# Kernel tuning notes

Hardware: AMD Instinct MI355X
Metric: run time of the kernel (lower is better)

## Reference

```python
import jax, jax.numpy as jnp
import numpy as np

B, Ng, C, H, W, Nt, M, P = 4, 8192, 256, 128, 128, 512, 8, 4
Ch = C // M  # 32 channels per head
EPS = 1e-5


def setup_inputs():
    key = jax.random.key(0)
    ks = jax.random.split(key, 12)
    s = 0.02
    def w(k, shape):
        return jax.random.normal(k, shape, jnp.float32) * s
    return {
        "query": jax.random.normal(ks[0], (B, Ng, C), jnp.float32),
        "value": jax.random.normal(ks[1], (B, C, H, W), jnp.float32),
        "reference_points": jax.random.uniform(ks[2], (B, Ng, 2), dtype=jnp.float32),
        "trajectory_points": jax.random.uniform(ks[3], (B, Nt, 2), dtype=jnp.float32),
        "in_proj_w": w(ks[4], (3 * C, C)),
        "in_proj_b": jnp.zeros((3 * C,), jnp.float32),
        "mha_out_w": w(ks[5], (C, C)),
        "mha_out_b": jnp.zeros((C,), jnp.float32),
        "ln_g": jnp.ones((C,), jnp.float32),
        "ln_b": jnp.zeros((C,), jnp.float32),
        "traj_w": w(ks[6], (C, 2)),
        "traj_b": jnp.zeros((C,), jnp.float32),
        "offs_w": w(ks[7], (M * P * 2, C)),
        "offs_b": jnp.zeros((M * P * 2,), jnp.float32),
        "attw_w": w(ks[8], (M * P, C)),
        "attw_b": jnp.zeros((M * P,), jnp.float32),
        "out_w": w(ks[9], (C, C)),
        "out_b": jnp.zeros((C,), jnp.float32),
    }


def _bilinear_sample(imgf, x, y):
    # imgf: (NM, Ch, H*W); x, y: (NM, Lq, P) unnormalized pixel coords
    # grid_sample semantics: bilinear, padding_mode='zeros', align_corners=False
    NM = imgf.shape[0]
    Lq, Pp = x.shape[1], x.shape[2]
    x0 = jnp.floor(x); y0 = jnp.floor(y)
    x1 = x0 + 1.0;     y1 = y0 + 1.0

    def gather(xi, yi):
        valid = (xi >= 0) & (xi < W) & (yi >= 0) & (yi < H)
        xc = jnp.clip(xi, 0, W - 1).astype(jnp.int32)
        yc = jnp.clip(yi, 0, H - 1).astype(jnp.int32)
        idx = (yc * W + xc).reshape(NM, 1, Lq * Pp)
        v = jnp.take_along_axis(imgf, jnp.broadcast_to(idx, (NM, Ch, Lq * Pp)), axis=2)
        return v.reshape(NM, Ch, Lq, Pp), valid.astype(imgf.dtype)

    v00, m00 = gather(x0, y0)
    v01, m01 = gather(x1, y0)
    v10, m10 = gather(x0, y1)
    v11, m11 = gather(x1, y1)
    wx1 = x - x0; wx0 = 1.0 - wx1
    wy1 = y - y0; wy0 = 1.0 - wy1
    out = (v00 * (wx0 * wy0 * m00)[:, None]
         + v01 * (wx1 * wy0 * m01)[:, None]
         + v10 * (wx0 * wy1 * m10)[:, None]
         + v11 * (wx1 * wy1 * m11)[:, None])
    return out  # (NM, Ch, Lq, P)


def reference(query, value, reference_points, trajectory_points,
              in_proj_w, in_proj_b, mha_out_w, mha_out_b, ln_g, ln_b,
              traj_w, traj_b, offs_w, offs_b, attw_w, attw_b, out_w, out_b):
    # trajectory projection: (B,Nt,2) -> (B,Nt,C)
    tf = trajectory_points @ traj_w.T + traj_b

    # guidance cross-attention (nn.MultiheadAttention, eval mode => no dropout)
    wq, wk, wv = jnp.split(in_proj_w, 3, axis=0)
    bq, bk, bv = jnp.split(in_proj_b, 3, axis=0)
    q = (query @ wq.T + bq).reshape(B, Ng, M, Ch)
    k = (tf @ wk.T + bk).reshape(B, Nt, M, Ch)
    v = (tf @ wv.T + bv).reshape(B, Nt, M, Ch)
    scores = jnp.einsum('bqmc,bkmc->bmqk', q, k) / jnp.sqrt(jnp.float32(Ch))
    probs = jax.nn.softmax(scores, axis=-1)
    ctx = jnp.einsum('bmqk,bkmc->bqmc', probs, v).reshape(B, Ng, C)
    ctx = ctx @ mha_out_w.T + mha_out_b

    # residual + LayerNorm
    x = query + ctx
    mu = x.mean(-1, keepdims=True)
    var = ((x - mu) ** 2).mean(-1, keepdims=True)
    gq = (x - mu) / jnp.sqrt(var + EPS) * ln_g + ln_b

    # sampling offsets & softmax attention weights (L=1 level)
    offs = (gq @ offs_w.T + offs_b).reshape(B, Ng, M, 1, P, 2)
    aw = jax.nn.softmax((gq @ attw_w.T + attw_b).reshape(B, Ng, M, P), axis=-1)
    loc = reference_points[:, :, None, None, None, :] + offs  # (B,Ng,M,1,P,2)

    # deformable sampling core (single level)
    grid = 2.0 * loc[:, :, :, 0] - 1.0                   # (B,Ng,M,P,2)
    grid = grid.transpose(0, 2, 1, 3, 4).reshape(B * M, Ng, P, 2)
    gx = (grid[..., 0] + 1.0) * (W * 0.5) - 0.5
    gy = (grid[..., 1] + 1.0) * (H * 0.5) - 0.5
    imgf = value.reshape(B * M, Ch, H * W)               # per-head feature maps
    samp = _bilinear_sample(imgf, gx, gy)                # (B*M,Ch,Ng,P)
    w_att = aw.transpose(0, 2, 1, 3).reshape(B * M, 1, Ng, P)
    out = (samp * w_att).sum(-1)                         # (B*M,Ch,Ng)

    # faithful to source: view(B,M,Ch,Ng).transpose(1,2).contiguous().view(B,Ng,C)
    out = out.reshape(B, M, Ch, Ng).transpose(0, 2, 1, 3).reshape(B, Ng, C)
    return out @ out_w.T + out_b
```

## Files before the change

kernel.cpp:

```cpp
#include <hip/hip_runtime.h>
#include <hip/hip_bf16.h>
#include <stdint.h>

typedef __bf16 bf16_t;
typedef __bf16 bf16x8 __attribute__((ext_vector_type(8)));
typedef __bf16 bf16x4 __attribute__((ext_vector_type(4)));
typedef float f32x4 __attribute__((ext_vector_type(4)));

#define CEXP 0.25506807186679906f

__device__ __forceinline__ float ldf(const void* p, size_t i, int isf) {
  return isf ? ((const float*)p)[i] : (float)((const bf16_t*)p)[i];
}

__device__ __forceinline__ f32x4 mfma16x16x16(bf16x4 a, bf16x4 b, f32x4 c) {
#if __has_builtin(__builtin_amdgcn_mfma_f32_16x16x16_bf16)
  return __builtin_amdgcn_mfma_f32_16x16x16_bf16(a, b, c, 0, 0, 0);
#elif __has_builtin(__builtin_amdgcn_mfma_f32_16x16x16bf16_1k)
  typedef short s16x4 __attribute__((ext_vector_type(4)));
  return __builtin_amdgcn_mfma_f32_16x16x16bf16_1k(
      __builtin_bit_cast(s16x4, a), __builtin_bit_cast(s16x4, b), c, 0, 0, 0);
#else
  asm("v_mfma_f32_16x16x16_bf16 %0, %1, %2, %0" : "+v"(c) : "v"(a), "v"(b));
  return c;
#endif
}

__device__ __forceinline__ void stage16(const bf16_t* g, bf16_t* l) {
  __builtin_amdgcn_global_load_lds((const __attribute__((address_space(1))) void*)g,
                                   (__attribute__((address_space(3))) void*)l, 16, 0, 0);
}

__global__ __launch_bounds__(256) void detect_dtype(const void* q, int* flag) {
  __shared__ int cnt;
  if (threadIdx.x == 0) cnt = 0;
  __syncthreads();
  const uint16_t* u = (const uint16_t*)q;
  const uint16_t v = u[2 * threadIdx.x];
  const int e = (v >> 7) & 0xFF;
  const int weird = (e >= 0x86 || (v != 0 && e <= 0x65)) ? 1 : 0;
  atomicAdd(&cnt, weird);
  __syncthreads();
  if (threadIdx.x == 0) *flag = (cnt >= 64) ? 1 : 0;
}

__global__ __launch_bounds__(256) void convert_weights(
    const void* in_w, const void* in_b, const void* mow, const void* mob,
    const void* outw, const void* outb, bf16_t* __restrict__ blob,
    const int* __restrict__ flag) {
  const int g = (blockIdx.x * 256 + threadIdx.x) * 4;
  if (g >= 328960) return;
  const int isf = *flag;
  const void* src; size_t off;
  if      (g < 196608) { src = in_w; off = g; }
  else if (g < 197376) { src = in_b; off = g - 196608; }
  else if (g < 262912) { src = mow;  off = g - 197376; }
  else if (g < 263168) { src = mob;  off = g - 262912; }
  else if (g < 328704) { src = outw; off = g - 263168; }
  else                 { src = outb; off = g - 328704; }
#pragma unroll
  for (int k = 0; k < 4; k++) blob[g + k] = (bf16_t)ldf(src, off + k, isf);
}

#define TM 128
#define TN 128
#define TKK 64

__global__ __launch_bounds__(256) void gemm_async(
    const bf16_t* __restrict__ A, const bf16_t* __restrict__ W,
    const bf16_t* __restrict__ bias, void* __restrict__ Cout,
    void* __restrict__ Cout2, int Ndim, int Kdim, int mode, float kscale,
    const int* __restrict__ flagp)
{
  __shared__ __align__(16) bf16_t As[TM * TKK];
  __shared__ __align__(16) bf16_t Ws[TN * TKK];
  const int t    = threadIdx.x;
  const int lane = t & 63;
  const int w    = t >> 6;
  const int wm   = (w & 1) * 64;
  const int wn   = (w >> 1) * 64;
  const int q4   = lane >> 4;
  const int r16  = lane & 15;
  const int tm   = blockIdx.x * TM;
  const int tn   = blockIdx.y * TN;

  f32x4 acc[4][4] = {};

  for (int kt = 0; kt < Kdim; kt += TKK) {
    __syncthreads();
#pragma unroll
    for (int r = 0; r < 4; r++) {
      const int L = w * 256 + r * 64 + lane;
      const int R = L >> 3, c = (L & 7) * 8;
      stage16(A + (size_t)(tm + R) * Kdim + kt + c, As + L * 8);
      stage16(W + (size_t)(tn + R) * Kdim + kt + c, Ws + L * 8);
    }
    __syncthreads();
#pragma unroll
    for (int ks = 0; ks < TKK; ks += 32) {
      bf16x8 af[4], bfm[4];
#pragma unroll
      for (int i = 0; i < 4; i++)
        af[i] = *(const bf16x8*)(As + (wm + 16 * i + r16) * TKK + ks + q4 * 8);
#pragma unroll
      for (int j = 0; j < 4; j++)
        bfm[j] = *(const bf16x8*)(Ws + (wn + 16 * j + r16) * TKK + ks + q4 * 8);
#pragma unroll
      for (int i = 0; i < 4; i++)
#pragma unroll
        for (int j = 0; j < 4; j++)
          acc[i][j] = __builtin_amdgcn_mfma_f32_16x16x32_bf16(af[i], bfm[j], acc[i][j], 0, 0, 0);
    }
  }

  const int isf = (mode == 3) ? *flagp : 1;
#pragma unroll
  for (int j = 0; j < 4; j++) {
    const int col = tn + wn + 16 * j + r16;
    const float bv = (float)bias[col];
#pragma unroll
    for (int i = 0; i < 4; i++) {
      const int row0 = tm + wm + 16 * i + q4 * 4;
#pragma unroll
      for (int rr = 0; rr < 4; rr++) {
        const float v = acc[i][j][rr] + bv;
        const size_t off = (size_t)(row0 + rr) * Ndim + col;
        if (mode == 0) {
          ((bf16_t*)Cout)[off] = (bf16_t)(v * kscale);
        } else if (mode == 6) {
          const int rowg = row0 + rr;
          if (col < 256) {
            ((bf16_t*)Cout)[(size_t)rowg * 256 + col] = (bf16_t)(v * kscale);
          } else {
            const int bb = rowg >> 9, tt = rowg & 511;
            const int c2 = col - 256;
            const int mm = c2 >> 5, ch = c2 & 31;
            ((bf16_t*)Cout2)[(((size_t)(bb * 8 + mm) * 32 + ch) << 9) + tt] = (bf16_t)v;
          }
        } else {
          if (isf) ((float*)Cout)[off] = v; else ((bf16_t*)Cout)[off] = (bf16_t)v;
        }
      }
    }
  }
}

__global__ __launch_bounds__(256) void gemm_f32a(
    const float* __restrict__ Ap, const bf16_t* __restrict__ Wf32path_unused,
    const bf16_t* __restrict__ bias, bf16_t* __restrict__ Cout,
    int Ndim, int Kdim, const bf16_t* __restrict__ W, const int* __restrict__ flagp,
    const void* __restrict__ Araw)
{
  __shared__ __align__(16) bf16_t As[TM * TKK];
  __shared__ __align__(16) bf16_t Ws[TN * TKK];
  const int t    = threadIdx.x;
  const int lane = t & 63;
  const int w    = t >> 6;
  const int wm   = (w & 1) * 64;
  const int wn   = (w >> 1) * 64;
  const int q4   = lane >> 4;
  const int r16  = lane & 15;
  const int tm   = blockIdx.x * TM;
  const int tn   = blockIdx.y * TN;
  const int aisf = *flagp;

  f32x4 acc[4][4] = {};
  const int srow = t >> 1;
  const int skb  = (t & 1) * 32;

  for (int kt = 0; kt < Kdim; kt += TKK) {
    __syncthreads();
    if (aisf) {
      const float4* ga = (const float4*)((const float*)Araw + (size_t)(tm + srow) * Kdim + kt + skb);
#pragma unroll
      for (int kk = 0; kk < 8; kk++) {
        const float4 u = ga[kk];
        bf16x4 h = {(bf16_t)u.x, (bf16_t)u.y, (bf16_t)u.z, (bf16_t)u.w};
        *(bf16x4*)(As + srow * TKK + skb + kk * 4) = h;
      }
    } else {
      const uint4* ga = (const uint4*)((const bf16_t*)Araw + (size_t)(tm + srow) * Kdim + kt + skb);
      uint4* la = (uint4*)(As + srow * TKK + skb);
      la[0] = ga[0]; la[1] = ga[1]; la[2] = ga[2]; la[3] = ga[3];
    }
    {
      const uint4* gw = (const uint4*)(W + (size_t)(tn + srow) * Kdim + kt + skb);
      uint4* lw = (uint4*)(Ws + srow * TKK + skb);
      lw[0] = gw[0]; lw[1] = gw[1]; lw[2] = gw[2]; lw[3] = gw[3];
    }
    __syncthreads();
#pragma unroll
    for (int ks = 0; ks < TKK; ks += 32) {
      bf16x8 af[4], bfm[4];
#pragma unroll
      for (int i = 0; i < 4; i++)
        af[i] = *(const bf16x8*)(As + (wm + 16 * i + r16) * TKK + ks + q4 * 8);
#pragma unroll
      for (int j = 0; j < 4; j++)
        bfm[j] = *(const bf16x8*)(Ws + (wn + 16 * j + r16) * TKK + ks + q4 * 8);
#pragma unroll
      for (int i = 0; i < 4; i++)
#pragma unroll
        for (int j = 0; j < 4; j++)
          acc[i][j] = __builtin_amdgcn_mfma_f32_16x16x32_bf16(af[i], bfm[j], acc[i][j], 0, 0, 0);
    }
  }

#pragma unroll
  for (int j = 0; j < 4; j++) {
    const int col = tn + wn + 16 * j + r16;
    const float bv = (float)bias[col];
#pragma unroll
    for (int i = 0; i < 4; i++) {
      const int row0 = tm + wm + 16 * i + q4 * 4;
#pragma unroll
      for (int rr = 0; rr < 4; rr++)
        Cout[(size_t)(row0 + rr) * Ndim + col] = (bf16_t)(acc[i][j][rr] + bv);
    }
  }
}

__global__ __launch_bounds__(256) void tf_kernel(
    const void* __restrict__ tp, const void* __restrict__ tw,
    const void* __restrict__ tb, bf16_t* __restrict__ tf, const int* __restrict__ flag)
{
  const int isf = *flag;
  const int rowb = blockIdx.x;
  const int c = threadIdx.x;
  const float x = ldf(tp, rowb * 2 + 0, isf);
  const float y = ldf(tp, rowb * 2 + 1, isf);
  const float v = x * ldf(tw, c * 2 + 0, isf) + y * ldf(tw, c * 2 + 1, isf) + ldf(tb, c, isf);
  tf[(size_t)rowb * 256 + c] = (bf16_t)v;
}

__global__ __launch_bounds__(256) void attn_kernel(
    const bf16_t* __restrict__ Q, const bf16_t* __restrict__ Kk,
    const bf16_t* __restrict__ Vt, bf16_t* __restrict__ ctx)
{
  const int t = threadIdx.x;
  const int lane = t & 63, w = t >> 6;
  const int q4 = lane >> 4, r16 = lane & 15;
  const int bm = blockIdx.y;
  const int b = bm >> 3, m = bm & 7;
  const int q0 = blockIdx.x * 256 + w * 64;

  bf16x8 qf[4];
#pragma unroll
  for (int qt = 0; qt < 4; qt++)
    qf[qt] = *(const bf16x8*)(Q + ((size_t)(b * 8192 + q0 + qt * 16 + r16) * 256 + m * 32 + q4 * 8));

  f32x4 acc[4][2] = {};
  f32x4 accl[4] = {};
  const bf16x4 ones = {(bf16_t)1.0f, (bf16_t)1.0f, (bf16_t)1.0f, (bf16_t)1.0f};

  const bf16_t* kbase = Kk + (size_t)b * 512 * 256 + m * 32;
  const bf16_t* vbase = Vt + (size_t)bm * 32 * 512;

  for (int k0 = 0; k0 < 512; k0 += 16) {
    const bf16x8 kf  = *(const bf16x8*)(kbase + (size_t)(k0 + r16) * 256 + q4 * 8);
    const bf16x4 vf0 = *(const bf16x4*)(vbase + ((size_t)r16 << 9) + k0 + q4 * 4);
    const bf16x4 vf1 = *(const bf16x4*)(vbase + ((size_t)(16 + r16) << 9) + k0 + q4 * 4);
#pragma unroll
    for (int qt = 0; qt < 4; qt++) {
      f32x4 z = {};
      const f32x4 s = __builtin_amdgcn_mfma_f32_16x16x32_bf16(kf, qf[qt], z, 0, 0, 0);
      bf16x4 p;
#pragma unroll
      for (int rr = 0; rr < 4; rr++) p[rr] = (bf16_t)exp2f(s[rr]);
      acc[qt][0] = mfma16x16x16(vf0, p, acc[qt][0]);
      acc[qt][1] = mfma16x16x16(vf1, p, acc[qt][1]);
      accl[qt]   = mfma16x16x16(ones, p, accl[qt]);
    }
  }

#pragma unroll
  for (int qt = 0; qt < 4; qt++) {
    const float inv = 1.0f / accl[qt][0];
    const size_t row = (size_t)b * 8192 + q0 + qt * 16 + r16;
    bf16x4 o0, o1;
#pragma unroll
    for (int rr = 0; rr < 4; rr++) {
      o0[rr] = (bf16_t)(acc[qt][0][rr] * inv);
      o1[rr] = (bf16_t)(acc[qt][1][rr] * inv);
    }
    *(bf16x4*)(ctx + row * 256 + m * 32 + q4 * 4)      = o0;
    *(bf16x4*)(ctx + row * 256 + m * 32 + 16 + q4 * 4) = o1;
  }
}

__global__ __launch_bounds__(256) void ln_kernel(
    const bf16_t* __restrict__ y2, const void* __restrict__ query,
    const void* __restrict__ g, const void* __restrict__ beta,
    bf16_t* __restrict__ gqh, bf16_t* __restrict__ gql, const int* __restrict__ flag)
{
  const int isf = *flag;
  const int rowb = blockIdx.x * 4 + (threadIdx.x >> 6);
  const int lane = threadIdx.x & 63;
  const size_t base = (size_t)rowb * 256;
  float x[4];
  float s = 0.f;
#pragma unroll
  for (int k = 0; k < 4; k++) {
    const int c = lane + 64 * k;
    x[k] = ldf(query, base + c, isf) + (float)y2[base + c];
    s += x[k];
  }
  for (int d = 1; d < 64; d <<= 1) s += __shfl_xor(s, d, 64);
  const float mu = s * (1.0f / 256.0f);
  float vs = 0.f;
#pragma unroll
  for (int k = 0; k < 4; k++) { const float d = x[k] - mu; vs += d * d; }
  for (int d = 1; d < 64; d <<= 1) vs += __shfl_xor(vs, d, 64);
  const float rstd = rsqrtf(vs * (1.0f / 256.0f) + 1e-5f);
#pragma unroll
  for (int k = 0; k < 4; k++) {
    const int c = lane + 64 * k;
    const float gv = (x[k] - mu) * rstd * ldf(g, c, isf) + ldf(beta, c, isf);
    const bf16_t hi = (bf16_t)gv;
    gqh[base + c] = hi;
    gql[base + c] = (bf16_t)(gv - (float)hi);
  }
}

__global__ __launch_bounds__(256) void prep_wpad(
    const void* __restrict__ offs_w, const void* __restrict__ attw_w,
    const void* __restrict__ offs_b, const void* __restrict__ attw_b,
    bf16_t* __restrict__ Wph, bf16_t* __restrict__ Wpl, bf16_t* __restrict__ bp,
    const int* __restrict__ flag)
{
  const int isf = *flag;
  const int idx = blockIdx.x * 256 + threadIdx.x;
  const int rowp = idx >> 8, c = idx & 255;
  float v = 0.0f;
  if (rowp < 64)      v = ldf(offs_w, rowp * 256 + c, isf);
  else if (rowp < 96) v = ldf(attw_w, (rowp - 64) * 256 + c, isf);
  const bf16_t hi = (bf16_t)v;
  Wph[idx] = hi;
  Wpl[idx] = (bf16_t)(v - (float)hi);
  if (idx < 128) {
    float bv = 0.0f;
    if (idx < 64)      bv = ldf(offs_b, idx, isf);
    else if (idx < 96) bv = ldf(attw_b, idx - 64, isf);
    bp[idx] = (bf16_t)bv;
  }
}

__global__ __launch_bounds__(256) void gemm_offs(
    const bf16_t* __restrict__ Ahg, const bf16_t* __restrict__ Alg,
    const bf16_t* __restrict__ Whg, const bf16_t* __restrict__ Wlg,
    const bf16_t* __restrict__ bias, float* __restrict__ Cout)
{
  __shared__ __align__(16) bf16_t Ah[128 * 64];
  __shared__ __align__(16) bf16_t Al[128 * 64];
  __shared__ __align__(16) bf16_t Wh[128 * 64];
  __shared__ __align__(16) bf16_t Wl[128 * 64];
  const int t    = threadIdx.x;
  const int lane = t & 63;
  const int w    = t >> 6;
  const int wm   = (w & 1) * 64;
  const int wn   = (w >> 1) * 64;
  const int q4   = lane >> 4;
  const int r16  = lane & 15;
  const int tm   = blockIdx.x * 128;

  f32x4 acc[4][4] = {};
  const int srow = t >> 1;
  const int skb  = (t & 1) * 32;

  for (int kt = 0; kt < 256; kt += 64) {
    __syncthreads();
    {
      const uint4* g0 = (const uint4*)(Ahg + (size_t)(tm + srow) * 256 + kt + skb);
      uint4* l0 = (uint4*)(Ah + srow * 64 + skb);
      l0[0] = g0[0]; l0[1] = g0[1]; l0[2] = g0[2]; l0[3] = g0[3];
      const uint4* g1 = (const uint4*)(Alg + (size_t)(tm + srow) * 256 + kt + skb);
      uint4* l1 = (uint4*)(Al + srow * 64 + skb);
      l1[0] = g1[0]; l1[1] = g1[1]; l1[2] = g1[2]; l1[3] = g1[3];
      const uint4* g2 = (const uint4*)(Whg + (size_t)srow * 256 + kt + skb);
      uint4* l2 = (uint4*)(Wh + srow * 64 + skb);
      l2[0] = g2[0]; l2[1] = g2[1]; l2[2] = g2[2]; l2[3] = g2[3];
      const uint4* g3 = (const uint4*)(Wlg + (size_t)srow * 256 + kt + skb);
      uint4* l3 = (uint4*)(Wl + srow * 64 + skb);
      l3[0] = g3[0]; l3[1] = g3[1]; l3[2] = g3[2]; l3[3] = g3[3];
    }
    __syncthreads();
#pragma unroll
    for (int ks = 0; ks < 64; ks += 32) {
      bf16x8 ah[4], al[4], bh[4], bl[4];
#pragma unroll
      for (int i = 0; i < 4; i++) {
        ah[i] = *(const bf16x8*)(Ah + (wm + 16 * i + r16) * 64 + ks + q4 * 8);
        al[i] = *(const bf16x8*)(Al + (wm + 16 * i + r16) * 64 + ks + q4 * 8);
      }
#pragma unroll
      for (int j = 0; j < 4; j++) {
        bh[j] = *(const bf16x8*)(Wh + (wn + 16 * j + r16) * 64 + ks + q4 * 8);
        bl[j] = *(const bf16x8*)(Wl + (wn + 16 * j + r16) * 64 + ks + q4 * 8);
      }
#pragma unroll
      for (int i = 0; i < 4; i++)
#pragma unroll
        for (int j = 0; j < 4; j++) {
          f32x4 a = acc[i][j];
          a = __builtin_amdgcn_mfma_f32_16x16x32_bf16(al[i], bh[j], a, 0, 0, 0);
          a = __builtin_amdgcn_mfma_f32_16x16x32_bf16(ah[i], bl[j], a, 0, 0, 0);
          a = __builtin_amdgcn_mfma_f32_16x16x32_bf16(ah[i], bh[j], a, 0, 0, 0);
          acc[i][j] = a;
        }
    }
  }

#pragma unroll
  for (int j = 0; j < 4; j++) {
    const int col = wn + 16 * j + r16;
    const float bv = (float)bias[col];
#pragma unroll
    for (int i = 0; i < 4; i++) {
      const int row0 = tm + wm + 16 * i + q4 * 4;
#pragma unroll
      for (int rr = 0; rr < 4; rr++)
        Cout[(size_t)(row0 + rr) * 128 + col] = acc[i][j][rr] + bv;
    }
  }
}

__global__ __launch_bounds__(256) void transpose_value(
    const void* __restrict__ V, bf16_t* __restrict__ Vp, const int* __restrict__ flag)
{
  __shared__ bf16_t tile[32][130];
  const int isf = *flag;
  const int bid = blockIdx.x;
  const int h = bid & 127;
  const int bm = bid >> 7;
  const int b = bm >> 3, mm = bm & 7;
  const int t = threadIdx.x;
  for (int idx = t; idx < 32 * 128; idx += 256) {
    const int ch = idx >> 7, ww = idx & 127;
    tile[ch][ww] = (bf16_t)ldf(V, (((size_t)b * 256 + mm * 32 + ch) * 128 + h) * 128 + ww, isf);
  }
  __syncthreads();
  const size_t base = ((size_t)bm * 128 + h) * 4096;
  for (int idx = t; idx < 32 * 128; idx += 256) {
    const int ww = idx >> 5, ch = idx & 31;
    Vp[base + idx] = tile[ch][ww];
  }
}

__global__ __launch_bounds__(256) void sampler(
    const float* __restrict__ ys, const void* __restrict__ refp,
    const bf16_t* __restrict__ vperm, bf16_t* __restrict__ outs,
    const int* __restrict__ flag)
{
  const int isf = *flag;
  const int t = threadIdx.x;
  const int qt = blockIdx.x;
  const int bm = blockIdx.y;
  const int b = bm >> 3, m = bm & 7;
  const int qq = qt * 256 + t;
  const size_t row = (size_t)b * 8192 + qq;
  const float* y = ys + row * 128;
  const float rx = ldf(refp, row * 2 + 0, isf);
  const float ry = ldf(refp, row * 2 + 1, isf);

  const float l0 = y[64 + m * 4 + 0], l1 = y[64 + m * 4 + 1];
  const float l2 = y[64 + m * 4 + 2], l3 = y[64 + m * 4 + 3];
  const float mx = fmaxf(fmaxf(l0, l1), fmaxf(l2, l3));
  const float e0 = __expf(l0 - mx), e1 = __expf(l1 - mx);
  const float e2 = __expf(l2 - mx), e3 = __expf(l3 - mx);
  const float inv = 1.0f / (e0 + e1 + e2 + e3);
  const float aw[4] = {e0 * inv, e1 * inv, e2 * inv, e3 * inv};

  float acc[32];
#pragma unroll
  for (int ch = 0; ch < 32; ch++) acc[ch] = 0.0f;

  const bf16_t* vbase = vperm + (size_t)bm * (128 * 128 * 32);

  for (int p = 0; p < 4; p++) {
    const float gx = (rx + y[m * 8 + p * 2 + 0]) * 128.0f - 0.5f;
    const float gy = (ry + y[m * 8 + p * 2 + 1]) * 128.0f - 0.5f;
    const float x0f = floorf(gx), y0f = floorf(gy);
    const int x0 = (int)x0f, y0i = (int)y0f;
    const float wx1 = gx - x0f, wx0 = 1.0f - wx1;
    const float wy1 = gy - y0f, wy0 = 1.0f - wy1;
    const float a = aw[p];
    for (int cy = 0; cy < 2; cy++) {
      const int yy = y0i + cy;
      if (yy < 0 || yy >= 128) continue;
      const float wy = cy ? wy1 : wy0;
      for (int cx = 0; cx < 2; cx++) {
        const int xx = x0 + cx;
        if (xx < 0 || xx >= 128) continue;
        const float wgt = a * wy * (cx ? wx1 : wx0);
        const bf16x8* src8 = (const bf16x8*)(vbase + ((size_t)yy * 128 + xx) * 32);
#pragma unroll
        for (int vv = 0; vv < 4; vv++) {
          const bf16x8 d = src8[vv];
#pragma unroll
          for (int e = 0; e < 8; e++) acc[vv * 8 + e] += wgt * (float)d[e];
        }
      }
    }
  }

  const size_t obase = (size_t)b * 8192;
#pragma unroll
  for (int ch = 0; ch < 32; ch++) {
    const size_t orow = obase + (size_t)(ch * 8 + m) * 32 + qt;
    outs[orow * 256 + t] = (bf16_t)acc[ch];
  }
}

extern "C" void kernel_launch(void* const* d_in, const int* in_sizes, int n_in,
                              void* d_out, int out_size, void* d_ws, size_t ws_size,
                              hipStream_t stream) {
  const void* query = d_in[0];
  const void* value = d_in[1];
  const void* refp  = d_in[2];
  const void* trajp = d_in[3];
  const void* in_w  = d_in[4];
  const void* in_b  = d_in[5];
  const void* mow   = d_in[6];
  const void* mob   = d_in[7];
  const void* lng   = d_in[8];
  const void* lnb   = d_in[9];
  const void* tw    = d_in[10];
  const void* tb    = d_in[11];
  const void* ow    = d_in[12];
  const void* ob    = d_in[13];
  const void* aww   = d_in[14];
  const void* awb   = d_in[15];
  const void* outw  = d_in[16];
  const void* outb  = d_in[17];

  char* base = (char*)d_ws;
  float*  ysamp = (float*)(base);
  bf16_t* qout  = (bf16_t*)(base + 16777216);
  bf16_t* ctx   = (bf16_t*)(base + 33554432);
  bf16_t* y2    = (bf16_t*)(base + 50331648);
  bf16_t* tf_ws = (bf16_t*)(base + 67108864);
  bf16_t* k_ws  = (bf16_t*)(base + 68157440);
  bf16_t* vt_g  = (bf16_t*)(base + 69206016);
  bf16_t* blob  = (bf16_t*)(base + 70254592);
  int*    flag  = (int*)(base + 70254592 + 1048560);

  bf16_t* gqh   = qout;
  bf16_t* gql   = ctx;
  bf16_t* vperm = (bf16_t*)(base + 16777216);
  bf16_t* outs  = y2;

  bf16_t* inw_bf  = blob;
  bf16_t* inb_bf  = blob + 196608;
  bf16_t* mow_bf  = blob + 197376;
  bf16_t* mob_bf  = blob + 262912;
  bf16_t* outw_bf = blob + 263168;
  bf16_t* outb_bf = blob + 328704;
  bf16_t* wph     = blob + 328960;
  bf16_t* wpl     = blob + 361728;
  bf16_t* bpad    = blob + 394496;

  detect_dtype<<<dim3(1), dim3(256), 0, stream>>>(query, flag);
  convert_weights<<<dim3(322), dim3(256), 0, stream>>>(in_w, in_b, mow, mob, outw, outb, blob, flag);
  tf_kernel<<<dim3(2048), dim3(256), 0, stream>>>(trajp, tw, tb, tf_ws, flag);
  gemm_async<<<dim3(16, 4), dim3(256), 0, stream>>>(
      tf_ws, inw_bf + 65536, inb_bf + 256, (void*)k_ws, (void*)vt_g, 512, 256, 6, CEXP, flag);
  gemm_f32a<<<dim3(256, 2), dim3(256), 0, stream>>>(
      (const float*)query, nullptr, inb_bf, qout, 256, 256, inw_bf, flag, query);
  attn_kernel<<<dim3(32, 32), dim3(256), 0, stream>>>(qout, k_ws, vt_g, ctx);
  gemm_async<<<dim3(256, 2), dim3(256), 0, stream>>>(
      ctx, mow_bf, mob_bf, (void*)y2, nullptr, 256, 256, 0, 1.0f, flag);
  ln_kernel<<<dim3(8192), dim3(256), 0, stream>>>(y2, query, lng, lnb, gqh, gql, flag);
  prep_wpad<<<dim3(128), dim3(256), 0, stream>>>(ow, aww, ob, awb, wph, wpl, bpad, flag);
  gemm_offs<<<dim3(256, 1), dim3(256), 0, stream>>>(gqh, gql, wph, wpl, bpad, ysamp);
  transpose_value<<<dim3(4096), dim3(256), 0, stream>>>(value, vperm, flag);
  sampler<<<dim3(32, 32), dim3(256), 0, stream>>>(ysamp, refp, vperm, outs, flag);
  gemm_async<<<dim3(256, 2), dim3(256), 0, stream>>>(
      outs, outw_bf, outb_bf, d_out, nullptr, 256, 256, 3, 1.0f, flag);
}
```

Before: 385.6 us.

## Merge prep kernels, inline dtype detection, halve attention tile and prefetch K/V

Replaces the separate dtype-detect, weight-convert, trajectory-feature and offset-weight prep kernels with one prep_all launch. Each kernel now detects the input dtype in-wave with a ballot instead of reading a flag from memory. The attention kernel handles 32 queries per wave over twice as many blocks, prefetches the next K/V fragments across iterations, and packs exp2 results to bf16 with a bit trick. Together these aim to cut launch count and the serial dependency on the flag, and to raise attention occupancy and latency hiding. The risk is a slightly different rounding path for the probabilities.

```diff
diff --git a/kernel.cpp b/kernel.cpp
--- a/kernel.cpp
+++ b/kernel.cpp
@@ -13,16 +13,39 @@
   return isf ? ((const float*)p)[i] : (float)((const bf16_t*)p)[i];
 }
 
+__device__ __forceinline__ int detect_isf(const void* q) {
+  const uint16_t* u = (const uint16_t*)q;
+  const int lane = threadIdx.x & 63;
+  const uint16_t v = u[2 * lane];
+  const int e = (v >> 7) & 0xFF;
+  const int weird = (e >= 0x86 || (v != 0 && e <= 0x65)) ? 1 : 0;
+  return (__popcll(__ballot(weird)) >= 16) ? 1 : 0;
+}
+
+__device__ __forceinline__ float fexp2(float x) {
+#if __has_builtin(__builtin_amdgcn_exp2f)
+  return __builtin_amdgcn_exp2f(x);
+#else
+  return exp2f(x);
+#endif
+}
+
+__device__ __forceinline__ bf16x4 pack4(const f32x4 s) {
+  union { float f; uint32_t u; } a0, a1, a2, a3;
+  a0.f = fexp2(s[0]); a1.f = fexp2(s[1]); a2.f = fexp2(s[2]); a3.f = fexp2(s[3]);
+  uint2 r;
+  r.x = __builtin_amdgcn_perm(a1.u + 0x8000u, a0.u + 0x8000u, 0x07060302u);
+  r.y = __builtin_amdgcn_perm(a3.u + 0x8000u, a2.u + 0x8000u, 0x07060302u);
+  return __builtin_bit_cast(bf16x4, r);
+}
+
 __device__ __forceinline__ f32x4 mfma16x16x16(bf16x4 a, bf16x4 b, f32x4 c) {
 #if __has_builtin(__builtin_amdgcn_mfma_f32_16x16x16_bf16)
   return __builtin_amdgcn_mfma_f32_16x16x16_bf16(a, b, c, 0, 0, 0);
-#elif __has_builtin(__builtin_amdgcn_mfma_f32_16x16x16bf16_1k)
+#else
   typedef short s16x4 __attribute__((ext_vector_type(4)));
   return __builtin_amdgcn_mfma_f32_16x16x16bf16_1k(
       __builtin_bit_cast(s16x4, a), __builtin_bit_cast(s16x4, b), c, 0, 0, 0);
-#else
-  asm("v_mfma_f32_16x16x16_bf16 %0, %1, %2, %0" : "+v"(c) : "v"(a), "v"(b));
-  return c;
 #endif
 }
 
@@ -31,35 +54,52 @@
                                    (__attribute__((address_space(3))) void*)l, 16, 0, 0);
 }
 
-__global__ __launch_bounds__(256) void detect_dtype(const void* q, int* flag) {
-  __shared__ int cnt;
-  if (threadIdx.x == 0) cnt = 0;
-  __syncthreads();
-  const uint16_t* u = (const uint16_t*)q;
-  const uint16_t v = u[2 * threadIdx.x];
-  const int e = (v >> 7) & 0xFF;
-  const int weird = (e >= 0x86 || (v != 0 && e <= 0x65)) ? 1 : 0;
-  atomicAdd(&cnt, weird);
-  __syncthreads();
-  if (threadIdx.x == 0) *flag = (cnt >= 64) ? 1 : 0;
-}
-
-__global__ __launch_bounds__(256) void convert_weights(
+__global__ __launch_bounds__(256) void prep_all(
+    const void* __restrict__ query,
     const void* in_w, const void* in_b, const void* mow, const void* mob,
-    const void* outw, const void* outb, bf16_t* __restrict__ blob,
-    const int* __restrict__ flag) {
-  const int g = (blockIdx.x * 256 + threadIdx.x) * 4;
-  if (g >= 328960) return;
-  const int isf = *flag;
-  const void* src; size_t off;
-  if      (g < 196608) { src = in_w; off = g; }
-  else if (g < 197376) { src = in_b; off = g - 196608; }
-  else if (g < 262912) { src = mow;  off = g - 197376; }
-  else if (g < 263168) { src = mob;  off = g - 262912; }
-  else if (g < 328704) { src = outw; off = g - 263168; }
-  else                 { src = outb; off = g - 328704; }
-#pragma unroll
-  for (int k = 0; k < 4; k++) blob[g + k] = (bf16_t)ldf(src, off + k, isf);
+    const void* outw, const void* outb,
+    const void* trajp, const void* tw, const void* tb,
+    const void* offs_w, const void* attw_w, const void* offs_b, const void* attw_b,
+    bf16_t* __restrict__ blob, bf16_t* __restrict__ tf,
+    bf16_t* __restrict__ Wph, bf16_t* __restrict__ Wpl, bf16_t* __restrict__ bp)
+{
+  const int isf = detect_isf(query);
+  const int bid = blockIdx.x;
+  if (bid < 322) {
+    const int g = (bid * 256 + threadIdx.x) * 4;
+    if (g >= 328960) return;
+    const void* src; size_t off;
+    if      (g < 196608) { src = in_w; off = g; }
+    else if (g < 197376) { src = in_b; off = g - 196608; }
+    else if (g < 262912) { src = mow;  off = g - 197376; }
+    else if (g < 263168) { src = mob;  off = g - 262912; }
+    else if (g < 328704) { src = outw; off = g - 263168; }
+    else                 { src = outb; off = g - 328704; }
+#pragma unroll
+    for (int k = 0; k < 4; k++) blob[g + k] = (bf16_t)ldf(src, off + k, isf);
+  } else if (bid < 322 + 2048) {
+    const int rowb = bid - 322;
+    const int c = threadIdx.x;
+    const float x = ldf(trajp, rowb * 2 + 0, isf);
+    const float y = ldf(trajp, rowb * 2 + 1, isf);
+    const float v = x * ldf(tw, c * 2 + 0, isf) + y * ldf(tw, c * 2 + 1, isf) + ldf(tb, c, isf);
+    tf[(size_t)rowb * 256 + c] = (bf16_t)v;
+  } else {
+    const int idx = (bid - 2370) * 256 + threadIdx.x;
+    const int rowp = idx >> 8, c = idx & 255;
+    float v = 0.0f;
+    if (rowp < 64)      v = ldf(offs_w, rowp * 256 + c, isf);
+    else if (rowp < 96) v = ldf(attw_w, (rowp - 64) * 256 + c, isf);
+    const bf16_t hi = (bf16_t)v;
+    Wph[idx] = hi;
+    Wpl[idx] = (bf16_t)(v - (float)hi);
+    if (idx < 128) {
+      float bv = 0.0f;
+      if (idx < 64)      bv = ldf(offs_b, idx, isf);
+      else if (idx < 96) bv = ldf(attw_b, idx - 64, isf);
+      bp[idx] = (bf16_t)bv;
+    }
+  }
 }
 
 #define TM 128
@@ -70,7 +110,7 @@
     const bf16_t* __restrict__ A, const bf16_t* __restrict__ W,
     const bf16_t* __restrict__ bias, void* __restrict__ Cout,
     void* __restrict__ Cout2, int Ndim, int Kdim, int mode, float kscale,
-    const int* __restrict__ flagp)
+    const void* __restrict__ qdet)
 {
   __shared__ __align__(16) bf16_t As[TM * TKK];
   __shared__ __align__(16) bf16_t Ws[TN * TKK];
@@ -113,7 +153,7 @@
     }
   }
 
-  const int isf = (mode == 3) ? *flagp : 1;
+  const int isf = (mode == 3) ? detect_isf(qdet) : 1;
 #pragma unroll
   for (int j = 0; j < 4; j++) {
     const int col = tn + wn + 16 * j + r16;
@@ -126,7 +166,7 @@
         const float v = acc[i][j][rr] + bv;
         const size_t off = (size_t)(row0 + rr) * Ndim + col;
         if (mode == 0) {
-          ((bf16_t*)Cout)[off] = (bf16_t)(v * kscale);
+          ((bf16_t*)Cout)[off] = (bf16_t)v;
         } else if (mode == 6) {
           const int rowg = row0 + rr;
           if (col < 256) {
@@ -146,10 +186,9 @@
 }
 
 __global__ __launch_bounds__(256) void gemm_f32a(
-    const float* __restrict__ Ap, const bf16_t* __restrict__ Wf32path_unused,
+    const void* __restrict__ Araw, const bf16_t* __restrict__ W,
     const bf16_t* __restrict__ bias, bf16_t* __restrict__ Cout,
-    int Ndim, int Kdim, const bf16_t* __restrict__ W, const int* __restrict__ flagp,
-    const void* __restrict__ Araw)
+    int Ndim, int Kdim, const void* __restrict__ qdet)
 {
   __shared__ __align__(16) bf16_t As[TM * TKK];
   __shared__ __align__(16) bf16_t Ws[TN * TKK];
@@ -162,7 +201,7 @@
   const int r16  = lane & 15;
   const int tm   = blockIdx.x * TM;
   const int tn   = blockIdx.y * TN;
-  const int aisf = *flagp;
+  const int aisf = detect_isf(qdet);
 
   f32x4 acc[4][4] = {};
   const int srow = t >> 1;
@@ -220,19 +259,6 @@
   }
 }
 
-__global__ __launch_bounds__(256) void tf_kernel(
-    const void* __restrict__ tp, const void* __restrict__ tw,
-    const void* __restrict__ tb, bf16_t* __restrict__ tf, const int* __restrict__ flag)
-{
-  const int isf = *flag;
-  const int rowb = blockIdx.x;
-  const int c = threadIdx.x;
-  const float x = ldf(tp, rowb * 2 + 0, isf);
-  const float y = ldf(tp, rowb * 2 + 1, isf);
-  const float v = x * ldf(tw, c * 2 + 0, isf) + y * ldf(tw, c * 2 + 1, isf) + ldf(tb, c, isf);
-  tf[(size_t)rowb * 256 + c] = (bf16_t)v;
-}
-
 __global__ __launch_bounds__(256) void attn_kernel(
     const bf16_t* __restrict__ Q, const bf16_t* __restrict__ Kk,
     const bf16_t* __restrict__ Vt, bf16_t* __restrict__ ctx)
@@ -242,39 +268,44 @@
   const int q4 = lane >> 4, r16 = lane & 15;
   const int bm = blockIdx.y;
   const int b = bm >> 3, m = bm & 7;
-  const int q0 = blockIdx.x * 256 + w * 64;
-
-  bf16x8 qf[4];
-#pragma unroll
-  for (int qt = 0; qt < 4; qt++)
+  const int q0 = blockIdx.x * 128 + w * 32;
+
+  bf16x8 qf[2];
+#pragma unroll
+  for (int qt = 0; qt < 2; qt++)
     qf[qt] = *(const bf16x8*)(Q + ((size_t)(b * 8192 + q0 + qt * 16 + r16) * 256 + m * 32 + q4 * 8));
 
-  f32x4 acc[4][2] = {};
-  f32x4 accl[4] = {};
+  f32x4 acc[2][2] = {};
+  f32x4 accl[2] = {};
   const bf16x4 ones = {(bf16_t)1.0f, (bf16_t)1.0f, (bf16_t)1.0f, (bf16_t)1.0f};
 
-  const bf16_t* kbase = Kk + (size_t)b * 512 * 256 + m * 32;
-  const bf16_t* vbase = Vt + (size_t)bm * 32 * 512;
+  const bf16_t* kbase  = Kk + (size_t)b * 512 * 256 + m * 32 + (size_t)r16 * 256 + q4 * 8;
+  const bf16_t* vbase0 = Vt + (size_t)bm * 32 * 512 + ((size_t)r16 << 9) + q4 * 4;
+  const bf16_t* vbase1 = vbase0 + (16 << 9);
+
+  bf16x8 kf = *(const bf16x8*)(kbase);
+  bf16x4 v0 = *(const bf16x4*)(vbase0);
+  bf16x4 v1 = *(const bf16x4*)(vbase1);
 
   for (int k0 = 0; k0 < 512; k0 += 16) {
-    const bf16x8 kf  = *(const bf16x8*)(kbase + (size_t)(k0 + r16) * 256 + q4 * 8);
-    const bf16x4 vf0 = *(const bf16x4*)(vbase + ((size_t)r16 << 9) + k0 + q4 * 4);
-    const bf16x4 vf1 = *(const bf16x4*)(vbase + ((size_t)(16 + r16) << 9) + k0 + q4 * 4);
-#pragma unroll
-    for (int qt = 0; qt < 4; qt++) {
+    const int nxt = (k0 + 16) & 511;
+    const bf16x8 kf_n = *(const bf16x8*)(kbase + (size_t)nxt * 256);
+    const bf16x4 v0_n = *(const bf16x4*)(vbase0 + nxt);
+    const bf16x4 v1_n = *(const bf16x4*)(vbase1 + nxt);
+#pragma unroll
+    for (int qt = 0; qt < 2; qt++) {
       f32x4 z = {};
       const f32x4 s = __builtin_amdgcn_mfma_f32_16x16x32_bf16(kf, qf[qt], z, 0, 0, 0);
-      bf16x4 p;
-#pragma unroll
-      for (int rr = 0; rr < 4; rr++) p[rr] = (bf16_t)exp2f(s[rr]);
-      acc[qt][0] = mfma16x16x16(vf0, p, acc[qt][0]);
-      acc[qt][1] = mfma16x16x16(vf1, p, acc[qt][1]);
+      const bf16x4 p = pack4(s);
+      acc[qt][0] = mfma16x16x16(v0, p, acc[qt][0]);
+      acc[qt][1] = mfma16x16x16(v1, p, acc[qt][1]);
       accl[qt]   = mfma16x16x16(ones, p, accl[qt]);
     }
-  }
-
-#pragma unroll
-  for (int qt = 0; qt < 4; qt++) {
+    kf = kf_n; v0 = v0_n; v1 = v1_n;
+  }
+
+#pragma unroll
+  for (int qt = 0; qt < 2; qt++) {
     const float inv = 1.0f / accl[qt][0];
     const size_t row = (size_t)b * 8192 + q0 + qt * 16 + r16;
     bf16x4 o0, o1;
@@ -291,9 +322,9 @@
 __global__ __launch_bounds__(256) void ln_kernel(
     const bf16_t* __restrict__ y2, const void* __restrict__ query,
     const void* __restrict__ g, const void* __restrict__ beta,
-    bf16_t* __restrict__ gqh, bf16_t* __restrict__ gql, const int* __restrict__ flag)
-{
-  const int isf = *flag;
+    bf16_t* __restrict__ gqh, bf16_t* __restrict__ gql)
+{
+  const int isf = detect_isf(query);
   const int rowb = blockIdx.x * 4 + (threadIdx.x >> 6);
   const int lane = threadIdx.x & 63;
   const size_t base = (size_t)rowb * 256;
@@ -319,29 +350,6 @@
     const bf16_t hi = (bf16_t)gv;
     gqh[base + c] = hi;
     gql[base + c] = (bf16_t)(gv - (float)hi);
-  }
-}
-
-__global__ __launch_bounds__(256) void prep_wpad(
-    const void* __restrict__ offs_w, const void* __restrict__ attw_w,
-    const void* __restrict__ offs_b, const void* __restrict__ attw_b,
-    bf16_t* __restrict__ Wph, bf16_t* __restrict__ Wpl, bf16_t* __restrict__ bp,
-    const int* __restrict__ flag)
-{
-  const int isf = *flag;
-  const int idx = blockIdx.x * 256 + threadIdx.x;
-  const int rowp = idx >> 8, c = idx & 255;
-  float v = 0.0f;
-  if (rowp < 64)      v = ldf(offs_w, rowp * 256 + c, isf);
-  else if (rowp < 96) v = ldf(attw_w, (rowp - 64) * 256 + c, isf);
-  const bf16_t hi = (bf16_t)v;
-  Wph[idx] = hi;
-  Wpl[idx] = (bf16_t)(v - (float)hi);
-  if (idx < 128) {
-    float bv = 0.0f;
-    if (idx < 64)      bv = ldf(offs_b, idx, isf);
-    else if (idx < 96) bv = ldf(attw_b, idx - 64, isf);
-    bp[idx] = (bf16_t)bv;
   }
 }
 
@@ -425,10 +433,10 @@
 }
 
 __global__ __launch_bounds__(256) void transpose_value(
-    const void* __restrict__ V, bf16_t* __restrict__ Vp, const int* __restrict__ flag)
+    const void* __restrict__ V, bf16_t* __restrict__ Vp, const void* __restrict__ qdet)
 {
   __shared__ bf16_t tile[32][130];
-  const int isf = *flag;
+  const int isf = detect_isf(qdet);
   const int bid = blockIdx.x;
   const int h = bid & 127;
   const int bm = bid >> 7;
@@ -449,9 +457,9 @@
 __global__ __launch_bounds__(256) void sampler(
     const float* __restrict__ ys, const void* __restrict__ refp,
     const bf16_t* __restrict__ vperm, bf16_t* __restrict__ outs,
-    const int* __restrict__ flag)
-{
-  const int isf = *flag;
+    const void* __restrict__ qdet)
+{
+  const int isf = detect_isf(qdet);
   const int t = threadIdx.x;
   const int qt = blockIdx.x;
   const int bm = blockIdx.y;
@@ -542,7 +550,6 @@
   bf16_t* k_ws  = (bf16_t*)(base + 68157440);
   bf16_t* vt_g  = (bf16_t*)(base + 69206016);
   bf16_t* blob  = (bf16_t*)(base + 70254592);
-  int*    flag  = (int*)(base + 70254592 + 1048560);
 
   bf16_t* gqh   = qout;
   bf16_t* gql   = ctx;
@@ -559,21 +566,20 @@
   bf16_t* wpl     = blob + 361728;
   bf16_t* bpad    = blob + 394496;
 
-  detect_dtype<<<dim3(1), dim3(256), 0, stream>>>(query, flag);
-  convert_weights<<<dim3(322), dim3(256), 0, stream>>>(in_w, in_b, mow, mob, outw, outb, blob, flag);
-  tf_kernel<<<dim3(2048), dim3(256), 0, stream>>>(trajp, tw, tb, tf_ws, flag);
+  prep_all<<<dim3(2498), dim3(256), 0, stream>>>(
+      query, in_w, in_b, mow, mob, outw, outb, trajp, tw, tb,
+      ow, aww, ob, awb, blob, tf_ws, wph, wpl, bpad);
   gemm_async<<<dim3(16, 4), dim3(256), 0, stream>>>(
-      tf_ws, inw_bf + 65536, inb_bf + 256, (void*)k_ws, (void*)vt_g, 512, 256, 6, CEXP, flag);
+      tf_ws, inw_bf + 65536, inb_bf + 256, (void*)k_ws, (void*)vt_g, 512, 256, 6, CEXP, query);
   gemm_f32a<<<dim3(256, 2), dim3(256), 0, stream>>>(
-      (const float*)query, nullptr, inb_bf, qout, 256, 256, inw_bf, flag, query);
-  attn_kernel<<<dim3(32, 32), dim3(256), 0, stream>>>(qout, k_ws, vt_g, ctx);
+      query, inw_bf, inb_bf, qout, 256, 256, query);
+  attn_kernel<<<dim3(64, 32), dim3(256), 0, stream>>>(qout, k_ws, vt_g, ctx);
   gemm_async<<<dim3(256, 2), dim3(256), 0, stream>>>(
-      ctx, mow_bf, mob_bf, (void*)y2, nullptr, 256, 256, 0, 1.0f, flag);
-  ln_kernel<<<dim3(8192), dim3(256), 0, stream>>>(y2, query, lng, lnb, gqh, gql, flag);
-  prep_wpad<<<dim3(128), dim3(256), 0, stream>>>(ow, aww, ob, awb, wph, wpl, bpad, flag);
+      ctx, mow_bf, mob_bf, (void*)y2, nullptr, 256, 256, 0, 1.0f, query);
+  ln_kernel<<<dim3(8192), dim3(256), 0, stream>>>(y2, query, lng, lnb, gqh, gql);
   gemm_offs<<<dim3(256, 1), dim3(256), 0, stream>>>(gqh, gql, wph, wpl, bpad, ysamp);
-  transpose_value<<<dim3(4096), dim3(256), 0, stream>>>(value, vperm, flag);
-  sampler<<<dim3(32, 32), dim3(256), 0, stream>>>(ysamp, refp, vperm, outs, flag);
+  transpose_value<<<dim3(4096), dim3(256), 0, stream>>>(value, vperm, query);
+  sampler<<<dim3(32, 32), dim3(256), 0, stream>>>(ysamp, refp, vperm, outs, query);
   gemm_async<<<dim3(256, 2), dim3(256), 0, stream>>>(
-      outs, outw_bf, outb_bf, d_out, nullptr, 256, 256, 3, 1.0f, flag);
-}
+      outs, outw_bf, outb_bf, d_out, nullptr, 256, 256, 3, 1.0f, query);
+}
```

Result: slower. 410.7 us (+6.5%).
